# Optimization experiments

Hardware: AMD Instinct MI355X
Metric: run time of the kernel (lower is better)

The kernel has to match this reference:

```python
import jax, jax.numpy as jnp
import numpy as np

TOPK = 8
MIN_TEMP = 0.5
NEG = -1e9  # finite stand-in for -inf (same softmax result, safe grads)


def setup_inputs() -> dict:
    key = jax.random.key(0)
    ks = jax.random.split(key, 6)
    B, S, D, N, K = 4, 4096, 1024, 256, 8
    token_states = jax.random.normal(ks[0], (B, S, D), dtype=jnp.float32)
    set_states = jax.random.normal(ks[1], (B, N, D), dtype=jnp.float32)
    desc_router = jax.random.normal(ks[2], (N, D), dtype=jnp.float32)
    token_to_sets = jax.random.randint(ks[3], (S, K), 0, N)
    Wq = jax.random.normal(ks[4], (D, D), dtype=jnp.float32) / np.sqrt(D)
    bq = jnp.zeros((D,), dtype=jnp.float32)
    temperature = jnp.ones((1,), dtype=jnp.float32)
    return {"token_states": token_states, "set_states": set_states,
            "desc_router": desc_router, "token_to_sets": token_to_sets,
            "Wq": Wq, "bq": bq, "temperature": temperature}


def reference(token_states, set_states, desc_router, token_to_sets, Wq, bq, temperature):
    B, S, D = token_states.shape
    N = set_states.shape[1]
    scale = 1.0 / np.sqrt(D)

    # q = Linear(token_states)
    q = jnp.einsum('bsd,ed->bse', token_states, Wq) + bq
    scores = jnp.einsum('bse,ne->bsn', q, desc_router) * scale  # [B,S,N]

    # restrict_to_sets: boolean routing mask built by scatter
    rows = jnp.broadcast_to(jnp.arange(S)[:, None], token_to_sets.shape)
    cols = jnp.clip(token_to_sets, 0, N - 1)
    valid = token_to_sets >= 0
    mask = jnp.zeros((S, N), dtype=bool).at[rows, cols].max(valid)
    scores = jnp.where(mask[None], scores, NEG)

    # top-k keep (topk < num_sets)
    topk_scores, topk_idx = jax.lax.top_k(scores, TOPK)
    b_idx = jnp.arange(B)[:, None, None]
    s_idx = jnp.arange(S)[None, :, None]
    keep = jnp.full_like(scores, NEG).at[b_idx, s_idx, topk_idx].set(topk_scores)

    temp = jnp.maximum(temperature, MIN_TEMP)  # clamp(min=0.5)
    weights = jax.nn.softmax(keep / temp, axis=-1)  # [B,S,N]
    token_repr = jnp.einsum('bsn,bnd->bsd', weights, set_states)
    bank_indices = jnp.argmax(weights, axis=-1)
    return token_repr, bank_indices, weights, topk_idx
```

## Files before the change

kernel.cpp:

```cpp
#include <hip/hip_runtime.h>
#include <math.h>
#include <float.h>


namespace {
constexpr int kB = 4, kS = 4096, kD = 1024, kN = 256, kK = 8;
constexpr float kScale = 0.03125f;
constexpr float kNeg = -1e9f;
constexpr float kLog2e = 1.4426950408889634f;
constexpr size_t kBankOff = (size_t)kB * kS * kD;
constexpr size_t kWOff    = kBankOff + (size_t)kB * kS;
constexpr size_t kTopkOff = kWOff + (size_t)kB * kS * kN;
constexpr int kEC = 8;
constexpr int kEL = kD / kEC;
constexpr int kNT = kN / 8;
}

#if __has_builtin(__builtin_amdgcn_exp2f)
#define FAST_EXP2(x) __builtin_amdgcn_exp2f(x)
#else
#define FAST_EXP2(x) exp2f(x)
#endif
#if __has_builtin(__builtin_amdgcn_rcpf)
#define FAST_RCP(x) __builtin_amdgcn_rcpf(x)
#else
#define FAST_RCP(x) (1.0f / (x))
#endif

__global__ __launch_bounds__(256) void k_prep(const float* __restrict__ dr,
                                              const float* __restrict__ wq,
                                              float* __restrict__ part) {
  const int nt = blockIdx.x, ec = blockIdx.y, t = threadIdx.x;
  const float4* wq4 = reinterpret_cast<const float4*>(wq);
  float4 acc[8];
#pragma unroll
  for (int j = 0; j < 8; ++j) acc[j] = make_float4(0.f, 0.f, 0.f, 0.f);
  const int e0 = ec * kEL;
#pragma unroll 4
  for (int e = e0; e < e0 + kEL; ++e) {
    const float4 wv = wq4[(size_t)e * (kD / 4) + t];
#pragma unroll
    for (int j = 0; j < 8; ++j) {
      const float a = dr[(size_t)(nt * 8 + j) * kD + e];
      acc[j].x += a * wv.x; acc[j].y += a * wv.y;
      acc[j].z += a * wv.z; acc[j].w += a * wv.w;
    }
  }
  float4* p4 = reinterpret_cast<float4*>(part);
#pragma unroll
  for (int j = 0; j < 8; ++j)
    p4[((size_t)ec * kN + nt * 8 + j) * (kD / 4) + t] = acc[j];
}

__global__ __launch_bounds__(256) void k_reduce(const float* __restrict__ part,
                                                const float* __restrict__ dr,
                                                const float* __restrict__ bq,
                                                float* __restrict__ R,
                                                float* __restrict__ bias) {
  const int n = blockIdx.x, t = threadIdx.x;
  const float4* p4 = reinterpret_cast<const float4*>(part);
  float4 a = make_float4(0.f, 0.f, 0.f, 0.f);
#pragma unroll
  for (int ec = 0; ec < kEC; ++ec) {
    const float4 p = p4[((size_t)ec * kN + n) * (kD / 4) + t];
    a.x += p.x; a.y += p.y; a.z += p.z; a.w += p.w;
  }
  a.x *= kScale; a.y *= kScale; a.z *= kScale; a.w *= kScale;
  reinterpret_cast<float4*>(R)[(size_t)n * (kD / 4) + t] = a;

  if (t < 64) {
    const float4* b4 = reinterpret_cast<const float4*>(bq);
    const float4* dr4 = reinterpret_cast<const float4*>(dr + (size_t)n * kD);
    float p = 0.f;
#pragma unroll
    for (int i = 0; i < 4; ++i) {
      const float4 bb = b4[t * 4 + i];
      const float4 dd = dr4[t * 4 + i];
      p += bb.x * dd.x + bb.y * dd.y + bb.z * dd.z + bb.w * dd.w;
    }
#pragma unroll
    for (int off = 32; off; off >>= 1) p += __shfl_xor(p, off);
    if (t == 0) bias[n] = p * kScale;
  }
}

__global__ __launch_bounds__(256) void k_score(const float* __restrict__ ts,
                                               const int* __restrict__ t2s,
                                               const float* __restrict__ R,
                                               const float* __restrict__ bias,
                                               const float* __restrict__ temp_p,
                                               int* __restrict__ st,
                                               float* __restrict__ out) {
  const int lane = threadIdx.x & 63;
  const int wid = threadIdx.x >> 6;
  const int bid = blockIdx.x;
  const int xcd = bid & 7;
  const int b = xcd >> 1;
  int s_ = ((bid >> 3) << 2) + wid + ((xcd & 1) << 11);
  const int s = __builtin_amdgcn_readfirstlane(s_);
  const size_t row = (size_t)b * kS + s;

  int nraw[kK], nk[kK];
#pragma unroll
  for (int k = 0; k < kK; ++k) {
    nraw[k] = t2s[s * kK + k];
    const int n = nraw[k];
    nk[k] = n < 0 ? 0 : (n > kN - 1 ? kN - 1 : n);
  }
  int validmask = 0;
#pragma unroll
  for (int k = 0; k < kK; ++k) {
    bool v = (nraw[k] >= 0);
#pragma unroll
    for (int j = 0; j < kK; ++j)
      if (j < k && nk[j] == nk[k]) v = false;
    validmask |= v ? (1 << k) : 0;
  }
  const int cnt = __popc(validmask);

  const float4* t4 = reinterpret_cast<const float4*>(ts) + row * (kD / 4);
  const float4 tv0 = t4[lane];
  const float4 tv1 = t4[64 + lane];
  const float4 tv2 = t4[128 + lane];
  const float4 tv3 = t4[192 + lane];

  float pk[kK];
#pragma unroll
  for (int k = 0; k < kK; ++k) {
    const float4* r4 = reinterpret_cast<const float4*>(R) + (size_t)nk[k] * (kD / 4);
    const float4 r0 = r4[lane];
    const float4 r1 = r4[64 + lane];
    const float4 r2 = r4[128 + lane];
    const float4 r3 = r4[192 + lane];
    float a = tv0.x * r0.x + tv0.y * r0.y + tv0.z * r0.z + tv0.w * r0.w;
    a += tv1.x * r1.x + tv1.y * r1.y + tv1.z * r1.z + tv1.w * r1.w;
    a += tv2.x * r2.x + tv2.y * r2.y + tv2.z * r2.z + tv2.w * r2.w;
    a += tv3.x * r3.x + tv3.y * r3.y + tv3.z * r3.z + tv3.w * r3.w;
    pk[k] = a;
  }
#pragma unroll
  for (int k = 0; k < kK; ++k) {
    float a = pk[k];
    a += __shfl_xor(a, 1);
    a += __shfl_xor(a, 2);
    a += __shfl_xor(a, 4);
    a += __shfl_xor(a, 8);
    a += __shfl_xor(a, 16);
    a += __shfl_xor(a, 32);
    pk[k] = a + bias[nk[k]];
  }

  unsigned long long pm0 = 0, pm1 = 0, pm2 = 0, pm3 = 0;
#pragma unroll
  for (int k = 0; k < kK; ++k) {
    const bool v = (validmask >> k) & 1;
    const unsigned long long bit = 1ull << (nk[k] & 63);
    const int wd = nk[k] >> 6;
    pm0 |= (v && wd == 0) ? bit : 0ull;
    pm1 |= (v && wd == 1) ? bit : 0ull;
    pm2 |= (v && wd == 2) ? bit : 0ull;
    pm3 |= (v && wd == 3) ? bit : 0ull;
  }
  int seq[kK];
#pragma unroll
  for (int i = 0; i < kK; ++i) {
    const unsigned long long i0 = ~pm0, i1 = ~pm1, i2 = ~pm2, i3 = ~pm3;
    const int c = i0 ? (__ffsll(i0) - 1)
                     : (i1 ? 64 + (__ffsll(i1) - 1)
                           : (i2 ? 128 + (__ffsll(i2) - 1)
                                 : 192 + (__ffsll(i3) - 1)));
    seq[i] = c;
    const unsigned long long b2 = 1ull << (c & 63);
    const int wd = c >> 6;
    pm0 |= (wd == 0) ? b2 : 0ull;
    pm1 |= (wd == 1) ? b2 : 0ull;
    pm2 |= (wd == 2) ? b2 : 0ull;
    pm3 |= (wd == 3) ? b2 : 0ull;
  }

  float fs[kK];
  int fi[kK];
#pragma unroll
  for (int k = 0; k < kK; ++k) {
    const bool v = (validmask >> k) & 1;
    const int jk = __popc((~validmask) & ((1 << k) - 1));
    int fv = seq[0];
#pragma unroll
    for (int j = 1; j < kK; ++j) fv = (jk == j) ? seq[j] : fv;
    fs[k] = v ? pk[k] : kNeg;
    fi[k] = v ? nk[k] : fv;
  }
#define CE(A, B)                                                        \
  {                                                                     \
    const bool sw = (fs[B] > fs[A]) || (fs[B] == fs[A] && fi[B] < fi[A]); \
    const float fa = fs[A], fb = fs[B];                                 \
    const int ia = fi[A], ib = fi[B];                                   \
    fs[A] = sw ? fb : fa; fs[B] = sw ? fa : fb;                         \
    fi[A] = sw ? ib : ia; fi[B] = sw ? ia : ib;                         \
  }
  CE(0,1) CE(2,3) CE(4,5) CE(6,7)
  CE(0,2) CE(1,3) CE(4,6) CE(5,7)
  CE(1,2) CE(5,6)
  CE(0,4) CE(1,5) CE(2,6) CE(3,7)
  CE(2,4) CE(3,5)
  CE(1,2) CE(3,4) CE(5,6)
#undef CE

  const float it = kLog2e * FAST_RCP(fmaxf(temp_p[0], 0.5f));
  float w[kK];
  float denom = 0.f;
#pragma unroll
  for (int i = 0; i < kK; ++i) {
    const float e = (i < cnt) ? FAST_EXP2((fs[i] - fs[0]) * it) : 0.f;
    w[i] = e;
    denom += e;
  }
  const float rd = FAST_RCP(denom);
#pragma unroll
  for (int i = 0; i < kK; ++i) w[i] *= rd;

  if (lane < kK) {
    int v = fi[0];
#pragma unroll
    for (int k = 1; k < kK; ++k) v = (lane == k) ? fi[k] : v;
    out[kTopkOff + row * kK + lane] = (float)v;
  }
  if (lane == 0) out[kBankOff + row] = (float)fi[0];

  int sel = 0;
#pragma unroll
  for (int k = 0; k < kK; ++k) {
    sel = (lane == k) ? __float_as_int(w[k]) : sel;
    sel = (lane == k + kK) ? fi[k] : sel;
  }
  if (lane < 16) st[row * 16 + lane] = sel;
}

__global__ __launch_bounds__(256) void k_repr(const float* __restrict__ ss,
                                              const int* __restrict__ st,
                                              float* __restrict__ out) {
  const int lane = threadIdx.x & 63;
  const int wid = threadIdx.x >> 6;
  const int bid = blockIdx.x;
  const int xcd = bid & 7;
  const int b = xcd >> 1;
  int s_ = ((bid >> 3) << 2) + wid + ((xcd & 1) << 11);
  const int s = __builtin_amdgcn_readfirstlane(s_);
  const size_t row = (size_t)b * kS + s;

  float w[kK];
  int fi[kK];
#pragma unroll
  for (int k = 0; k < kK; ++k) {
    w[k] = __int_as_float(st[row * 16 + k]);
    fi[k] = st[row * 16 + kK + k];
  }

  const float4* ssb = reinterpret_cast<const float4*>(ss) + (size_t)b * kN * (kD / 4);
  float4* o4 = reinterpret_cast<float4*>(out) + row * (kD / 4);
#pragma unroll
  for (int c = 0; c < 4; ++c) {
    float4 v0 = ssb[(size_t)fi[0] * (kD / 4) + c * 64 + lane];
    float4 v1 = ssb[(size_t)fi[1] * (kD / 4) + c * 64 + lane];
    float4 v2 = ssb[(size_t)fi[2] * (kD / 4) + c * 64 + lane];
    float4 v3 = ssb[(size_t)fi[3] * (kD / 4) + c * 64 + lane];
    float4 v4 = ssb[(size_t)fi[4] * (kD / 4) + c * 64 + lane];
    float4 v5 = ssb[(size_t)fi[5] * (kD / 4) + c * 64 + lane];
    float4 v6 = ssb[(size_t)fi[6] * (kD / 4) + c * 64 + lane];
    float4 v7 = ssb[(size_t)fi[7] * (kD / 4) + c * 64 + lane];
    float4 acc;
    acc.x = w[0] * v0.x + w[1] * v1.x + w[2] * v2.x + w[3] * v3.x
          + w[4] * v4.x + w[5] * v5.x + w[6] * v6.x + w[7] * v7.x;
    acc.y = w[0] * v0.y + w[1] * v1.y + w[2] * v2.y + w[3] * v3.y
          + w[4] * v4.y + w[5] * v5.y + w[6] * v6.y + w[7] * v7.y;
    acc.z = w[0] * v0.z + w[1] * v1.z + w[2] * v2.z + w[3] * v3.z
          + w[4] * v4.z + w[5] * v5.z + w[6] * v6.z + w[7] * v7.z;
    acc.w = w[0] * v0.w + w[1] * v1.w + w[2] * v2.w + w[3] * v3.w
          + w[4] * v4.w + w[5] * v5.w + w[6] * v6.w + w[7] * v7.w;
    o4[c * 64 + lane] = acc;
  }

  {
    const int cb = lane * 4;
    float4 wv = make_float4(0.f, 0.f, 0.f, 0.f);
#pragma unroll
    for (int k = 0; k < kK; ++k) {
      wv.x = (fi[k] == cb    ) ? w[k] : wv.x;
      wv.y = (fi[k] == cb + 1) ? w[k] : wv.y;
      wv.z = (fi[k] == cb + 2) ? w[k] : wv.z;
      wv.w = (fi[k] == cb + 3) ? w[k] : wv.w;
    }
    reinterpret_cast<float4*>(out + kWOff)[row * (kN / 4) + lane] = wv;
  }
}

extern "C" void kernel_launch(void* const* d_in, const int* in_sizes, int n_in,
                              void* d_out, int out_size, void* d_ws, size_t ws_size,
                              hipStream_t stream) {
  const float* ts  = (const float*)d_in[0];
  const float* ss  = (const float*)d_in[1];
  const float* dr  = (const float*)d_in[2];
  const int*   t2s = (const int*)  d_in[3];
  const float* wq  = (const float*)d_in[4];
  const float* bq  = (const float*)d_in[5];
  const float* tmp = (const float*)d_in[6];
  float* out = (float*)d_out;

  float* R    = (float*)d_ws;
  float* bias = R + (size_t)kN * kD;
  int*   st   = (int*)(bias + kN);
  float* part = out + kWOff;

  k_prep<<<dim3(kNT, kEC), 256, 0, stream>>>(dr, wq, part);
  k_reduce<<<kN, 256, 0, stream>>>(part, dr, bq, R, bias);
  k_score<<<kB * kS / 4, 256, 0, stream>>>(ts, t2s, R, bias, tmp, st, out);
  k_repr<<<kB * kS / 4, 256, 0, stream>>>(ss, st, out);
}
```

Baseline: 81.27 us.

## Process all batches of a token per wave in k_score to share routing and R loads

Restructures k_score so that each wavefront handles one sequence position across all four batches, with 16 lanes per batch, instead of one (batch, position) row per wave. The routing-index decode, dedup and the gathered R rows are now shared across batches, which cuts redundant t2s and R traffic and shortens the cross-lane reduction to four shuffle steps. The grid shrinks by a factor of four and the old XCD-aware block remapping is dropped. The dot product becomes a 16-step loop with eight accumulators, and launch bounds request higher occupancy, which raises register pressure per lane.

```diff
diff --git a/kernel.cpp b/kernel.cpp
--- a/kernel.cpp
+++ b/kernel.cpp
@@ -84,21 +84,18 @@
   }
 }
 
-__global__ __launch_bounds__(256) void k_score(const float* __restrict__ ts,
-                                               const int* __restrict__ t2s,
-                                               const float* __restrict__ R,
-                                               const float* __restrict__ bias,
-                                               const float* __restrict__ temp_p,
-                                               int* __restrict__ st,
-                                               float* __restrict__ out) {
+__global__ __launch_bounds__(256, 4) void k_score(const float* __restrict__ ts,
+                                                  const int* __restrict__ t2s,
+                                                  const float* __restrict__ R,
+                                                  const float* __restrict__ bias,
+                                                  const float* __restrict__ temp_p,
+                                                  int* __restrict__ st,
+                                                  float* __restrict__ out) {
   const int lane = threadIdx.x & 63;
   const int wid = threadIdx.x >> 6;
-  const int bid = blockIdx.x;
-  const int xcd = bid & 7;
-  const int b = xcd >> 1;
-  int s_ = ((bid >> 3) << 2) + wid + ((xcd & 1) << 11);
-  const int s = __builtin_amdgcn_readfirstlane(s_);
-  const size_t row = (size_t)b * kS + s;
+  const int u = lane & 15;
+  const int g = lane >> 4;
+  const int s = __builtin_amdgcn_readfirstlane(blockIdx.x * 4 + wid);
 
   int nraw[kK], nk[kK];
 #pragma unroll
@@ -118,35 +115,30 @@
   }
   const int cnt = __popc(validmask);
 
-  const float4* t4 = reinterpret_cast<const float4*>(ts) + row * (kD / 4);
-  const float4 tv0 = t4[lane];
-  const float4 tv1 = t4[64 + lane];
-  const float4 tv2 = t4[128 + lane];
-  const float4 tv3 = t4[192 + lane];
+  const float4* ts4 = reinterpret_cast<const float4*>(ts);
+  const float4* R4 = reinterpret_cast<const float4*>(R);
+  const size_t tbase = ((size_t)g * kS + s) * (kD / 4) + u;
+  float acc[kK];
+#pragma unroll
+  for (int k = 0; k < kK; ++k) acc[k] = 0.f;
+#pragma unroll 2
+  for (int i = 0; i < 16; ++i) {
+    const float4 tv = ts4[tbase + i * 16];
+#pragma unroll
+    for (int k = 0; k < kK; ++k) {
+      const float4 rv = R4[(size_t)nk[k] * (kD / 4) + i * 16 + u];
+      acc[k] += tv.x * rv.x + tv.y * rv.y + tv.z * rv.z + tv.w * rv.w;
+    }
+  }
 
   float pk[kK];
 #pragma unroll
   for (int k = 0; k < kK; ++k) {
-    const float4* r4 = reinterpret_cast<const float4*>(R) + (size_t)nk[k] * (kD / 4);
-    const float4 r0 = r4[lane];
-    const float4 r1 = r4[64 + lane];
-    const float4 r2 = r4[128 + lane];
-    const float4 r3 = r4[192 + lane];
-    float a = tv0.x * r0.x + tv0.y * r0.y + tv0.z * r0.z + tv0.w * r0.w;
-    a += tv1.x * r1.x + tv1.y * r1.y + tv1.z * r1.z + tv1.w * r1.w;
-    a += tv2.x * r2.x + tv2.y * r2.y + tv2.z * r2.z + tv2.w * r2.w;
-    a += tv3.x * r3.x + tv3.y * r3.y + tv3.z * r3.z + tv3.w * r3.w;
-    pk[k] = a;
-  }
-#pragma unroll
-  for (int k = 0; k < kK; ++k) {
-    float a = pk[k];
+    float a = acc[k];
     a += __shfl_xor(a, 1);
     a += __shfl_xor(a, 2);
     a += __shfl_xor(a, 4);
     a += __shfl_xor(a, 8);
-    a += __shfl_xor(a, 16);
-    a += __shfl_xor(a, 32);
     pk[k] = a + bias[nk[k]];
   }
 
@@ -219,21 +211,22 @@
 #pragma unroll
   for (int i = 0; i < kK; ++i) w[i] *= rd;
 
-  if (lane < kK) {
+  const size_t row = (size_t)g * kS + s;
+  if (u < kK) {
     int v = fi[0];
 #pragma unroll
-    for (int k = 1; k < kK; ++k) v = (lane == k) ? fi[k] : v;
-    out[kTopkOff + row * kK + lane] = (float)v;
-  }
-  if (lane == 0) out[kBankOff + row] = (float)fi[0];
+    for (int k = 1; k < kK; ++k) v = (u == k) ? fi[k] : v;
+    out[kTopkOff + row * kK + u] = (float)v;
+  }
+  if (u == 0) out[kBankOff + row] = (float)fi[0];
 
   int sel = 0;
 #pragma unroll
   for (int k = 0; k < kK; ++k) {
-    sel = (lane == k) ? __float_as_int(w[k]) : sel;
-    sel = (lane == k + kK) ? fi[k] : sel;
-  }
-  if (lane < 16) st[row * 16 + lane] = sel;
+    sel = (u == k) ? __float_as_int(w[k]) : sel;
+    sel = (u == k + kK) ? fi[k] : sel;
+  }
+  st[row * 16 + u] = sel;
 }
 
 __global__ __launch_bounds__(256) void k_repr(const float* __restrict__ ss,
@@ -313,6 +306,6 @@
 
   k_prep<<<dim3(kNT, kEC), 256, 0, stream>>>(dr, wq, part);
   k_reduce<<<kN, 256, 0, stream>>>(part, dr, bq, R, bias);
-  k_score<<<kB * kS / 4, 256, 0, stream>>>(ts, t2s, R, bias, tmp, st, out);
+  k_score<<<kS / 4, 256, 0, stream>>>(ts, t2s, R, bias, tmp, st, out);
   k_repr<<<kB * kS / 4, 256, 0, stream>>>(ss, st, out);
 }
```

New measurement: 77.80 us. 1.04x faster.
